# Optimization experiments

Measured on AMD Instinct MI355X. Metric: run time of the kernel, lower is better.

The kernel has to match this reference:

```python
import jax, jax.numpy as jnp
import numpy as np
from jax import lax

PADLEN = 9  # 3 * max(len(a), len(b)) for an order-2 filter (3 taps each)


def _butter2_lowpass(cutoff, fs):
    # 2nd-order Butterworth lowpass via bilinear transform; matches
    # scipy.signal.butter(2, 2*cutoff/fs, btype='lowpass', output='ba')
    c = 1.0 / np.tan(np.pi * cutoff / fs)
    a0 = 1.0 + np.sqrt(2.0) * c + c * c
    b = np.array([1.0, 2.0, 1.0]) / a0
    a = np.array([a0, 2.0 - 2.0 * c * c, 1.0 - np.sqrt(2.0) * c + c * c]) / a0
    return b.astype(np.float32), a.astype(np.float32)


def setup_inputs() -> dict:
    key = jax.random.key(0)
    x = jax.random.normal(key, (16, 64, 48000), dtype=jnp.float32)
    b, a = _butter2_lowpass(1000.0, 48000.0)
    return {"x": x, "b": jnp.asarray(b), "a": jnp.asarray(a)}


def _pad_odd(x, n):
    # Odd-reflection padding, identical to _BaseFilter._pad_odd
    left_end = x[..., 0:1]
    left_ext = jnp.flip(x[..., 0:n], axis=-1)
    right_end = x[..., -1:]
    right_ext = jnp.flip(x[..., -(n + 2):-2], axis=-1)
    return jnp.concatenate((2.0 * left_end - left_ext, x, 2.0 * right_end - right_ext), axis=-1)


def _lfilter(x, a, b):
    # x: (N, T). Direct-form II transposed IIR with zero initial conditions
    # (same semantics as torchaudio.functional.lfilter, clamp=False).
    a0 = a[0]
    a_n = a / a0
    b_n = b / a0
    order = a.shape[0] - 1
    b0 = b_n[0]
    b_rest = b_n[1:]  # (order,)
    a_rest = a_n[1:]  # (order,)

    def step(z, xt):
        # z: (N, order) filter state, xt: (N,)
        y = b0 * xt + z[:, 0]
        z_new = xt[:, None] * b_rest - y[:, None] * a_rest
        z_new = z_new.at[:, :-1].add(z[:, 1:])
        return z_new, y

    z0 = jnp.zeros((x.shape[0], order), x.dtype)
    _, y = lax.scan(step, z0, x.T)  # y: (T, N)
    return y.T


def _filtfilt(x, a, b):
    # torchaudio.functional.filtfilt: forward lfilter (clamp=False), then
    # reversed lfilter with clamp=True (default), then reverse.
    fwd = _lfilter(x, a, b)
    bwd = _lfilter(jnp.flip(fwd, axis=-1), a, b)
    return jnp.clip(jnp.flip(bwd, axis=-1), -1.0, 1.0)


def reference(x, b, a):
    shape = x.shape
    scale = jnp.max(jnp.abs(x), axis=-1, keepdims=True)
    xn = x / scale
    xp = _pad_odd(xn, PADLEN)                     # (..., T + 2*PADLEN)
    x2 = xp.reshape(-1, xp.shape[-1])             # flatten lanes for the scan
    y2 = _filtfilt(x2, a, b)
    y = y2.reshape(shape[:-1] + (y2.shape[-1],))
    y = y[..., PADLEN:-PADLEN]                    # unpad back to T
    return y * scale
```

## Files before the change

kernel.cpp:

```cpp
#include <hip/hip_runtime.h>

#define NROWS 1024
#define N     48000
#define PAD   9
#define NPADE (N + PAD)

#define CL  8
#define W   512
#define GR  2
#define WU  80
#define MW  352
#define NB  138
#define NPR 69
#define WPB 2
#define NBLK (NROWS * NPR / WPB)

typedef float v4f __attribute__((ext_vector_type(4)));

#define SWZ(g) (((g) & ~7) | (((g) & 7) ^ (((g) >> 3) & 7)))

__device__ __forceinline__ float rfl(float v) {
    return __int_as_float(__builtin_amdgcn_readfirstlane(__float_as_int(v)));
}

__device__ __forceinline__ float xt_fetch(const float* __restrict__ xr, int t) {
    if (t < -PAD || t >= NPADE) return 0.0f;
    if (t < 0)  return 2.0f * xr[0]     - xr[-1 - t];
    if (t < N)  return xr[t];
    return 2.0f * xr[N - 1] - xr[2 * N - 3 - t];
}

#define FS(px,py,pz,pw,d) { float l0 = __shfl_up(s0, d), l1 = __shfl_up(s1, d);   \
    if (lane >= d) { s0 = fmaf(px, l0, fmaf(py, l1, s0));                         \
                     s1 = fmaf(pz, l0, fmaf(pw, l1, s1)); } }
#define BS(px,py,pz,pw,d) { float l0 = __shfl_down(s0, d), l1 = __shfl_down(s1, d);\
    if (lane < 64 - d) { s0 = fmaf(px, l0, fmaf(py, l1, s0));                     \
                         s1 = fmaf(pz, l0, fmaf(pw, l1, s1)); } }

#define SQR() { float t00 = m00*m00 + m01*m10, t01 = m00*m01 + m01*m11;           \
                float t10 = m10*m00 + m11*m10, t11 = m10*m01 + m11*m11;           \
                m00 = t00; m01 = t01; m10 = t10; m11 = t11; }

__device__ __forceinline__ void prefetch_win(const float* __restrict__ src,
                                             int lane_swz,
                                             float* __restrict__ slice) {
    #pragma unroll
    for (int m = 0; m < GR; ++m) {
        __builtin_amdgcn_global_load_lds(
            (const __attribute__((address_space(1))) float*)(src + 4 * (m * 64 + lane_swz)),
            (__attribute__((address_space(3))) float*)(slice + 4 * (m * 64)),
            16, 0, 0);
    }
}

__global__ __launch_bounds__(128, 8) void filt_kernel(
    const float* __restrict__ x,
    const float* __restrict__ bc,
    const float* __restrict__ ac,
    float* __restrict__ out)
{
    __shared__ float lds[WPB][2][W];

    const int lane = threadIdx.x & 63;
    const int wid  = threadIdx.x >> 6;
    const unsigned w = blockIdx.x * WPB + wid;
    const unsigned r = w / (unsigned)NPR;
    const unsigned j = w - r * (unsigned)NPR;
    const int tb0a = (int)(2 * j)     * MW - WU;
    const int tb0b = (int)(2 * j + 1) * MW - WU;
    const int lane_swz = (lane & ~7) | ((lane & 7) ^ ((lane >> 3) & 7));

    const float b0  = rfl(bc[0]), b1 = rfl(bc[1]), b2 = rfl(bc[2]);
    const float na1 = rfl(-ac[1]), na2 = rfl(-ac[2]);
    const float* xr = x + (size_t)r * N;
    float* orow = out + (size_t)r * N;

    float m00 = na1, m01 = 1.f, m10 = na2, m11 = 0.f;
    SQR() SQR() SQR()
    const float p0x=rfl(m00), p0y=rfl(m01), p0z=rfl(m10), p0w=rfl(m11); SQR()
    const float p1x=rfl(m00), p1y=rfl(m01), p1z=rfl(m10), p1w=rfl(m11); SQR()
    const float p2x=rfl(m00), p2y=rfl(m01), p2z=rfl(m10), p2w=rfl(m11); SQR()
    const float p3x=rfl(m00), p3y=rfl(m01), p3z=rfl(m10), p3w=rfl(m11);

    const bool intA = (tb0a >= 0) && (tb0a + W <= N);
    const bool intB = (tb0b + W <= N);

    if (intA) prefetch_win(xr + tb0a, lane_swz, &lds[wid][0][0]);
    if (intB) prefetch_win(xr + tb0b, lane_swz, &lds[wid][1][0]);

    auto process_win = [&](float* wbuf, int tb0, bool interior) {
        const int tb = tb0 + lane * CL;

        if (!interior) {
            #pragma unroll
            for (int m = 0; m < GR; ++m) {
                int g = m * 64 + lane;
                int t = tb0 + 4 * g;
                *(float4*)(wbuf + 4 * SWZ(g)) =
                    make_float4(xt_fetch(xr, t),     xt_fetch(xr, t + 1),
                                xt_fetch(xr, t + 2), xt_fetch(xr, t + 3));
            }
        }

        float c[CL];
        #pragma unroll
        for (int m = 0; m < CL / 4; ++m) {
            float4 v = *(const float4*)(wbuf + 4 * SWZ(2 * lane + m));
            int kk = 4 * m;
            c[kk] = v.x; c[kk+1] = v.y; c[kk+2] = v.z; c[kk+3] = v.w;
        }

        float xm1 = 0.f, xm2 = 0.f, ym1 = 0.f, ym2 = 0.f;
        #pragma unroll
        for (int k = 0; k < CL; ++k) {
            float xk = c[k];
            float X  = fmaf(b1, xm1, b2 * xm2);
            X        = fmaf(b0, xk, X);
            float p  = fmaf(na2, ym2, X);
            float y  = fmaf(na1, ym1, p);
            c[k] = y;
            xm2 = xm1; xm1 = xk; ym2 = ym1; ym1 = y;
        }
        float s0 = fmaf(b1, xm1, b2 * xm2);
        s0 = fmaf(na1, ym1, s0); s0 = fmaf(na2, ym2, s0);
        float s1 = fmaf(na2, ym1, b2 * xm1);

        FS(p0x,p0y,p0z,p0w, 1) FS(p1x,p1y,p1z,p1w, 2)
        FS(p2x,p2y,p2z,p2w, 4) FS(p3x,p3y,p3z,p3w, 8)
        float in0 = __shfl_up(s0, 1), in1 = __shfl_up(s1, 1);
        if (lane == 0) { in0 = 0.f; in1 = 0.f; }

        {
            float hm = in0;
            float h  = fmaf(na1, in0, in1);
            c[0] += hm;
            #pragma unroll
            for (int k = 1; k < CL; ++k) {
                c[k] += h;
                float nh = fmaf(na1, h, na2 * hm);
                hm = h; h = nh;
            }
        }

        if (tb + CL > NPADE) {
            #pragma unroll
            for (int k = 0; k < CL; ++k)
                if (tb + k >= NPADE) c[k] = 0.f;
        }

        xm1 = 0.f; xm2 = 0.f; ym1 = 0.f; ym2 = 0.f;
        #pragma unroll
        for (int k = CL - 1; k >= 0; --k) {
            float xk = c[k];
            float X  = fmaf(b1, xm1, b2 * xm2);
            X        = fmaf(b0, xk, X);
            float p  = fmaf(na2, ym2, X);
            float y  = fmaf(na1, ym1, p);
            c[k] = y;
            xm2 = xm1; xm1 = xk; ym2 = ym1; ym1 = y;
        }
        s0 = fmaf(b1, xm1, b2 * xm2);
        s0 = fmaf(na1, ym1, s0); s0 = fmaf(na2, ym2, s0);
        s1 = fmaf(na2, ym1, b2 * xm1);

        BS(p0x,p0y,p0z,p0w, 1) BS(p1x,p1y,p1z,p1w, 2)
        BS(p2x,p2y,p2z,p2w, 4) BS(p3x,p3y,p3z,p3w, 8)
        in0 = __shfl_down(s0, 1); in1 = __shfl_down(s1, 1);
        if (lane == 63) { in0 = 0.f; in1 = 0.f; }

        {
            float hm = in0;
            float h  = fmaf(na1, in0, in1);
            c[CL - 1] += hm;
            #pragma unroll
            for (int k = CL - 2; k >= 0; --k) {
                c[k] += h;
                float nh = fmaf(na1, h, na2 * hm);
                hm = h; h = nh;
            }
        }

        #pragma unroll
        for (int m = 0; m < CL / 4; ++m) {
            int kk = 4 * m;
            *(float4*)(wbuf + 4 * SWZ(2 * lane + m)) =
                make_float4(c[kk], c[kk+1], c[kk+2], c[kk+3]);
        }
        #pragma unroll
        for (int m = 0; m < GR; ++m) {
            int g = m * 64 + lane;
            int t = tb0 + 4 * g;
            if (g >= WU / 4 && g < (WU + MW) / 4 && t + 4 <= N) {
                v4f v = *(const v4f*)(wbuf + 4 * (m * 64 + lane_swz));
                __builtin_nontemporal_store(v, (v4f*)(orow + t));
            }
        }
    };

    if (intA) {
        if (intB) asm volatile("s_waitcnt vmcnt(2)" ::: "memory");
        else      asm volatile("s_waitcnt vmcnt(0)" ::: "memory");
    }
    process_win(&lds[wid][0][0], tb0a, intA);

    if (intB) asm volatile("s_waitcnt vmcnt(2)" ::: "memory");
    process_win(&lds[wid][1][0], tb0b, intB);
}

extern "C" void kernel_launch(void* const* d_in, const int* in_sizes, int n_in,
                              void* d_out, int out_size, void* d_ws, size_t ws_size,
                              hipStream_t stream) {
    const float* x  = (const float*)d_in[0];
    const float* bc = (const float*)d_in[1];
    const float* ac = (const float*)d_in[2];
    float* out = (float*)d_out;

    filt_kernel<<<dim3(NBLK), dim3(128), 0, stream>>>(x, bc, ac, out);
}
```

Measured before the change: 71.68 us.

## Process four windows per wave with two independent chains interleaved for ILP

Each wave now covers four overlapping windows instead of two, prefetching all four into LDS up front and processing them in pairs. Within each pair the forward/backward recurrences and shuffle-based scans are interleaved, so two independent dependency chains hide FMA and cross-lane shuffle latency. Prefetch addresses are clamped so the async loads are always issued, with edge windows restaged afterwards. The cost is more LDS per block and more registers (launch bounds occupancy hint lowered to 5), which cuts resident waves.

Measured after the change: 70.63 us. About the same (-1.5%).

```diff
diff --git a/kernel.cpp b/kernel.cpp
--- a/kernel.cpp
+++ b/kernel.cpp
@@ -10,10 +10,9 @@
 #define GR  2
 #define WU  80
 #define MW  352
-#define NB  138
-#define NPR 69
+#define NQ  35
 #define WPB 2
-#define NBLK (NROWS * NPR / WPB)
+#define NBLK (NROWS * NQ / WPB)
 
 typedef float v4f __attribute__((ext_vector_type(4)));
 
@@ -30,12 +29,18 @@
     return 2.0f * xr[N - 1] - xr[2 * N - 3 - t];
 }
 
-#define FS(px,py,pz,pw,d) { float l0 = __shfl_up(s0, d), l1 = __shfl_up(s1, d);   \
-    if (lane >= d) { s0 = fmaf(px, l0, fmaf(py, l1, s0));                         \
-                     s1 = fmaf(pz, l0, fmaf(pw, l1, s1)); } }
-#define BS(px,py,pz,pw,d) { float l0 = __shfl_down(s0, d), l1 = __shfl_down(s1, d);\
-    if (lane < 64 - d) { s0 = fmaf(px, l0, fmaf(py, l1, s0));                     \
-                         s1 = fmaf(pz, l0, fmaf(pw, l1, s1)); } }
+#define FS2(px,py,pz,pw,d)                                                        \
+  { float la0 = __shfl_up(s0a, d), la1 = __shfl_up(s1a, d);                       \
+    float lb0 = __shfl_up(s0b, d), lb1 = __shfl_up(s1b, d);                       \
+    if (lane >= d) {                                                              \
+      s0a = fmaf(px, la0, fmaf(py, la1, s0a)); s1a = fmaf(pz, la0, fmaf(pw, la1, s1a)); \
+      s0b = fmaf(px, lb0, fmaf(py, lb1, s0b)); s1b = fmaf(pz, lb0, fmaf(pw, lb1, s1b)); } }
+#define BS2(px,py,pz,pw,d)                                                        \
+  { float la0 = __shfl_down(s0a, d), la1 = __shfl_down(s1a, d);                   \
+    float lb0 = __shfl_down(s0b, d), lb1 = __shfl_down(s1b, d);                   \
+    if (lane < 64 - d) {                                                          \
+      s0a = fmaf(px, la0, fmaf(py, la1, s0a)); s1a = fmaf(pz, la0, fmaf(pw, la1, s1a)); \
+      s0b = fmaf(px, lb0, fmaf(py, lb1, s0b)); s1b = fmaf(pz, lb0, fmaf(pw, lb1, s1b)); } }
 
 #define SQR() { float t00 = m00*m00 + m01*m10, t01 = m00*m01 + m01*m11;           \
                 float t10 = m10*m00 + m11*m10, t11 = m10*m01 + m11*m11;           \
@@ -53,21 +58,23 @@
     }
 }
 
-__global__ __launch_bounds__(128, 8) void filt_kernel(
+__global__ __launch_bounds__(128, 5) void filt_kernel(
     const float* __restrict__ x,
     const float* __restrict__ bc,
     const float* __restrict__ ac,
     float* __restrict__ out)
 {
-    __shared__ float lds[WPB][2][W];
+    __shared__ float lds[WPB][4][W];
 
     const int lane = threadIdx.x & 63;
     const int wid  = threadIdx.x >> 6;
     const unsigned w = blockIdx.x * WPB + wid;
-    const unsigned r = w / (unsigned)NPR;
-    const unsigned j = w - r * (unsigned)NPR;
-    const int tb0a = (int)(2 * j)     * MW - WU;
-    const int tb0b = (int)(2 * j + 1) * MW - WU;
+    const unsigned r = w / (unsigned)NQ;
+    const unsigned q = w - r * (unsigned)NQ;
+    const int tb0A = (int)(4 * q)     * MW - WU;
+    const int tb0B = (int)(4 * q + 1) * MW - WU;
+    const int tb0C = (int)(4 * q + 2) * MW - WU;
+    const int tb0D = (int)(4 * q + 3) * MW - WU;
     const int lane_swz = (lane & ~7) | ((lane & 7) ^ ((lane >> 3) & 7));
 
     const float b0  = rfl(bc[0]), b1 = rfl(bc[1]), b2 = rfl(bc[2]);
@@ -82,129 +89,159 @@
     const float p2x=rfl(m00), p2y=rfl(m01), p2z=rfl(m10), p2w=rfl(m11); SQR()
     const float p3x=rfl(m00), p3y=rfl(m01), p3z=rfl(m10), p3w=rfl(m11);
 
-    const bool intA = (tb0a >= 0) && (tb0a + W <= N);
-    const bool intB = (tb0b + W <= N);
-
-    if (intA) prefetch_win(xr + tb0a, lane_swz, &lds[wid][0][0]);
-    if (intB) prefetch_win(xr + tb0b, lane_swz, &lds[wid][1][0]);
-
-    auto process_win = [&](float* wbuf, int tb0, bool interior) {
-        const int tb = tb0 + lane * CL;
-
-        if (!interior) {
-            #pragma unroll
-            for (int m = 0; m < GR; ++m) {
-                int g = m * 64 + lane;
-                int t = tb0 + 4 * g;
-                *(float4*)(wbuf + 4 * SWZ(g)) =
-                    make_float4(xt_fetch(xr, t),     xt_fetch(xr, t + 1),
-                                xt_fetch(xr, t + 2), xt_fetch(xr, t + 3));
-            }
-        }
-
-        float c[CL];
-        #pragma unroll
-        for (int m = 0; m < CL / 4; ++m) {
-            float4 v = *(const float4*)(wbuf + 4 * SWZ(2 * lane + m));
-            int kk = 4 * m;
-            c[kk] = v.x; c[kk+1] = v.y; c[kk+2] = v.z; c[kk+3] = v.w;
-        }
-
-        float xm1 = 0.f, xm2 = 0.f, ym1 = 0.f, ym2 = 0.f;
-        #pragma unroll
-        for (int k = 0; k < CL; ++k) {
-            float xk = c[k];
-            float X  = fmaf(b1, xm1, b2 * xm2);
-            X        = fmaf(b0, xk, X);
-            float p  = fmaf(na2, ym2, X);
-            float y  = fmaf(na1, ym1, p);
-            c[k] = y;
-            xm2 = xm1; xm1 = xk; ym2 = ym1; ym1 = y;
-        }
-        float s0 = fmaf(b1, xm1, b2 * xm2);
-        s0 = fmaf(na1, ym1, s0); s0 = fmaf(na2, ym2, s0);
-        float s1 = fmaf(na2, ym1, b2 * xm1);
-
-        FS(p0x,p0y,p0z,p0w, 1) FS(p1x,p1y,p1z,p1w, 2)
-        FS(p2x,p2y,p2z,p2w, 4) FS(p3x,p3y,p3z,p3w, 8)
-        float in0 = __shfl_up(s0, 1), in1 = __shfl_up(s1, 1);
-        if (lane == 0) { in0 = 0.f; in1 = 0.f; }
-
-        {
-            float hm = in0;
-            float h  = fmaf(na1, in0, in1);
-            c[0] += hm;
-            #pragma unroll
-            for (int k = 1; k < CL; ++k) {
-                c[k] += h;
-                float nh = fmaf(na1, h, na2 * hm);
-                hm = h; h = nh;
-            }
-        }
-
-        if (tb + CL > NPADE) {
-            #pragma unroll
-            for (int k = 0; k < CL; ++k)
-                if (tb + k >= NPADE) c[k] = 0.f;
-        }
-
-        xm1 = 0.f; xm2 = 0.f; ym1 = 0.f; ym2 = 0.f;
-        #pragma unroll
-        for (int k = CL - 1; k >= 0; --k) {
-            float xk = c[k];
-            float X  = fmaf(b1, xm1, b2 * xm2);
-            X        = fmaf(b0, xk, X);
-            float p  = fmaf(na2, ym2, X);
-            float y  = fmaf(na1, ym1, p);
-            c[k] = y;
-            xm2 = xm1; xm1 = xk; ym2 = ym1; ym1 = y;
-        }
-        s0 = fmaf(b1, xm1, b2 * xm2);
-        s0 = fmaf(na1, ym1, s0); s0 = fmaf(na2, ym2, s0);
-        s1 = fmaf(na2, ym1, b2 * xm1);
-
-        BS(p0x,p0y,p0z,p0w, 1) BS(p1x,p1y,p1z,p1w, 2)
-        BS(p2x,p2y,p2z,p2w, 4) BS(p3x,p3y,p3z,p3w, 8)
-        in0 = __shfl_down(s0, 1); in1 = __shfl_down(s1, 1);
-        if (lane == 63) { in0 = 0.f; in1 = 0.f; }
-
-        {
-            float hm = in0;
-            float h  = fmaf(na1, in0, in1);
-            c[CL - 1] += hm;
-            #pragma unroll
-            for (int k = CL - 2; k >= 0; --k) {
-                c[k] += h;
-                float nh = fmaf(na1, h, na2 * hm);
-                hm = h; h = nh;
-            }
-        }
-
-        #pragma unroll
-        for (int m = 0; m < CL / 4; ++m) {
-            int kk = 4 * m;
-            *(float4*)(wbuf + 4 * SWZ(2 * lane + m)) =
-                make_float4(c[kk], c[kk+1], c[kk+2], c[kk+3]);
-        }
+    const bool inA = (tb0A >= 0) && (tb0A + W <= N);
+    const bool inB = (tb0B >= 0) && (tb0B + W <= N);
+    const bool inC = (tb0C >= 0) && (tb0C + W <= N);
+    const bool inD = (tb0D >= 0) && (tb0D + W <= N);
+    const bool acA = (tb0A + WU < N), acB = (tb0B + WU < N);
+    const bool acC = (tb0C + WU < N), acD = (tb0D + WU < N);
+
+    #define CLAMP(t) (min(max((t), 0), N - W))
+    prefetch_win(xr + CLAMP(tb0A), lane_swz, &lds[wid][0][0]);
+    prefetch_win(xr + CLAMP(tb0B), lane_swz, &lds[wid][1][0]);
+    prefetch_win(xr + CLAMP(tb0C), lane_swz, &lds[wid][2][0]);
+    prefetch_win(xr + CLAMP(tb0D), lane_swz, &lds[wid][3][0]);
+
+    auto stage_edge = [&](float* wbuf, int tb0) {
         #pragma unroll
         for (int m = 0; m < GR; ++m) {
             int g = m * 64 + lane;
             int t = tb0 + 4 * g;
-            if (g >= WU / 4 && g < (WU + MW) / 4 && t + 4 <= N) {
+            *(float4*)(wbuf + 4 * SWZ(g)) =
+                make_float4(xt_fetch(xr, t),     xt_fetch(xr, t + 1),
+                            xt_fetch(xr, t + 2), xt_fetch(xr, t + 3));
+        }
+    };
+
+    auto pp = [&](float* bufa, int ta, bool ia, float* bufb, int tb_, bool ib) {
+        if (!ia) stage_edge(bufa, ta);
+        if (!ib) stage_edge(bufb, tb_);
+
+        float ca[CL], cb[CL];
+        #pragma unroll
+        for (int m = 0; m < CL / 4; ++m) {
+            float4 va = *(const float4*)(bufa + 4 * SWZ(2 * lane + m));
+            float4 vb = *(const float4*)(bufb + 4 * SWZ(2 * lane + m));
+            int kk = 4 * m;
+            ca[kk] = va.x; ca[kk+1] = va.y; ca[kk+2] = va.z; ca[kk+3] = va.w;
+            cb[kk] = vb.x; cb[kk+1] = vb.y; cb[kk+2] = vb.z; cb[kk+3] = vb.w;
+        }
+
+        float x1a=0.f,x2a=0.f,y1a=0.f,y2a=0.f;
+        float x1b=0.f,x2b=0.f,y1b=0.f,y2b=0.f;
+        #pragma unroll
+        for (int k = 0; k < CL; ++k) {
+            float xa = ca[k], xb = cb[k];
+            float Xa = fmaf(b0, xa, fmaf(b1, x1a, b2 * x2a));
+            float Xb = fmaf(b0, xb, fmaf(b1, x1b, b2 * x2b));
+            float ya = fmaf(na1, y1a, fmaf(na2, y2a, Xa));
+            float yb = fmaf(na1, y1b, fmaf(na2, y2b, Xb));
+            ca[k] = ya; cb[k] = yb;
+            x2a = x1a; x1a = xa; y2a = y1a; y1a = ya;
+            x2b = x1b; x1b = xb; y2b = y1b; y1b = yb;
+        }
+        float s0a = fmaf(na2, y2a, fmaf(na1, y1a, fmaf(b1, x1a, b2 * x2a)));
+        float s1a = fmaf(na2, y1a, b2 * x1a);
+        float s0b = fmaf(na2, y2b, fmaf(na1, y1b, fmaf(b1, x1b, b2 * x2b)));
+        float s1b = fmaf(na2, y1b, b2 * x1b);
+
+        FS2(p0x,p0y,p0z,p0w, 1) FS2(p1x,p1y,p1z,p1w, 2)
+        FS2(p2x,p2y,p2z,p2w, 4) FS2(p3x,p3y,p3z,p3w, 8)
+        float i0a = __shfl_up(s0a, 1), i1a = __shfl_up(s1a, 1);
+        float i0b = __shfl_up(s0b, 1), i1b = __shfl_up(s1b, 1);
+        if (lane == 0) { i0a = 0.f; i1a = 0.f; i0b = 0.f; i1b = 0.f; }
+
+        {
+            float hma = i0a, ha = fmaf(na1, i0a, i1a);
+            float hmb = i0b, hb = fmaf(na1, i0b, i1b);
+            ca[0] += hma; cb[0] += hmb;
+            #pragma unroll
+            for (int k = 1; k < CL; ++k) {
+                ca[k] += ha; cb[k] += hb;
+                float nha = fmaf(na1, ha, na2 * hma);
+                float nhb = fmaf(na1, hb, na2 * hmb);
+                hma = ha; ha = nha; hmb = hb; hb = nhb;
+            }
+        }
+
+        const int tba = ta + lane * CL, tbb = tb_ + lane * CL;
+        if (tba + CL > NPADE) {
+            #pragma unroll
+            for (int k = 0; k < CL; ++k) if (tba + k >= NPADE) ca[k] = 0.f;
+        }
+        if (tbb + CL > NPADE) {
+            #pragma unroll
+            for (int k = 0; k < CL; ++k) if (tbb + k >= NPADE) cb[k] = 0.f;
+        }
+
+        x1a=0.f; x2a=0.f; y1a=0.f; y2a=0.f;
+        x1b=0.f; x2b=0.f; y1b=0.f; y2b=0.f;
+        #pragma unroll
+        for (int k = CL - 1; k >= 0; --k) {
+            float xa = ca[k], xb = cb[k];
+            float Xa = fmaf(b0, xa, fmaf(b1, x1a, b2 * x2a));
+            float Xb = fmaf(b0, xb, fmaf(b1, x1b, b2 * x2b));
+            float ya = fmaf(na1, y1a, fmaf(na2, y2a, Xa));
+            float yb = fmaf(na1, y1b, fmaf(na2, y2b, Xb));
+            ca[k] = ya; cb[k] = yb;
+            x2a = x1a; x1a = xa; y2a = y1a; y1a = ya;
+            x2b = x1b; x1b = xb; y2b = y1b; y1b = yb;
+        }
+        s0a = fmaf(na2, y2a, fmaf(na1, y1a, fmaf(b1, x1a, b2 * x2a)));
+        s1a = fmaf(na2, y1a, b2 * x1a);
+        s0b = fmaf(na2, y2b, fmaf(na1, y1b, fmaf(b1, x1b, b2 * x2b)));
+        s1b = fmaf(na2, y1b, b2 * x1b);
+
+        BS2(p0x,p0y,p0z,p0w, 1) BS2(p1x,p1y,p1z,p1w, 2)
+        BS2(p2x,p2y,p2z,p2w, 4) BS2(p3x,p3y,p3z,p3w, 8)
+        i0a = __shfl_down(s0a, 1); i1a = __shfl_down(s1a, 1);
+        i0b = __shfl_down(s0b, 1); i1b = __shfl_down(s1b, 1);
+        if (lane == 63) { i0a = 0.f; i1a = 0.f; i0b = 0.f; i1b = 0.f; }
+
+        {
+            float hma = i0a, ha = fmaf(na1, i0a, i1a);
+            float hmb = i0b, hb = fmaf(na1, i0b, i1b);
+            ca[CL - 1] += hma; cb[CL - 1] += hmb;
+            #pragma unroll
+            for (int k = CL - 2; k >= 0; --k) {
+                ca[k] += ha; cb[k] += hb;
+                float nha = fmaf(na1, ha, na2 * hma);
+                float nhb = fmaf(na1, hb, na2 * hmb);
+                hma = ha; ha = nha; hmb = hb; hb = nhb;
+            }
+        }
+
+        #pragma unroll
+        for (int m = 0; m < CL / 4; ++m) {
+            int kk = 4 * m;
+            *(float4*)(bufa + 4 * SWZ(2 * lane + m)) =
+                make_float4(ca[kk], ca[kk+1], ca[kk+2], ca[kk+3]);
+            *(float4*)(bufb + 4 * SWZ(2 * lane + m)) =
+                make_float4(cb[kk], cb[kk+1], cb[kk+2], cb[kk+3]);
+        }
+    };
+
+    auto store_win = [&](float* wbuf, int tb0, bool act) {
+        if (!act) return;
+        #pragma unroll
+        for (int m = 0; m < GR; ++m) {
+            int g = m * 64 + lane;
+            int t = tb0 + 4 * g;
+            if (g >= WU / 4 && g < (WU + MW) / 4 && t >= 0 && t + 4 <= N) {
                 v4f v = *(const v4f*)(wbuf + 4 * (m * 64 + lane_swz));
                 __builtin_nontemporal_store(v, (v4f*)(orow + t));
             }
         }
     };
 
-    if (intA) {
-        if (intB) asm volatile("s_waitcnt vmcnt(2)" ::: "memory");
-        else      asm volatile("s_waitcnt vmcnt(0)" ::: "memory");
-    }
-    process_win(&lds[wid][0][0], tb0a, intA);
-
-    if (intB) asm volatile("s_waitcnt vmcnt(2)" ::: "memory");
-    process_win(&lds[wid][1][0], tb0b, intB);
+    asm volatile("s_waitcnt vmcnt(4)" ::: "memory");
+    pp(&lds[wid][0][0], tb0A, inA, &lds[wid][1][0], tb0B, inB);
+    asm volatile("s_waitcnt vmcnt(0)" ::: "memory");
+    store_win(&lds[wid][0][0], tb0A, acA);
+    store_win(&lds[wid][1][0], tb0B, acB);
+    pp(&lds[wid][2][0], tb0C, inC, &lds[wid][3][0], tb0D, inD);
+    store_win(&lds[wid][2][0], tb0C, acC);
+    store_win(&lds[wid][3][0], tb0D, acD);
 }
 
 extern "C" void kernel_launch(void* const* d_in, const int* in_sizes, int n_in,
```
